# Optimization experiments

Hardware: AMD Instinct MI355X
Metric: run time of the kernel (lower is better)

Reference implementation:

```python
import jax, jax.numpy as jnp
import numpy as np
import math

B, T, S, D, H = 64, 128, 3, 1024, 8
DK = D // H  # 128


def setup_inputs() -> dict:
    key = jax.random.key(0)
    ks = jax.random.split(key, 12)
    sc = 0.02
    inputs = jax.random.normal(ks[0], (B, T, D), jnp.float32)
    # init_memory: identity over slots, zero-padded to d_model, flattened
    memory = jnp.broadcast_to(jnp.eye(S, D, dtype=jnp.float32), (B, S, D)).reshape(B, S * D)
    def lin(k, din, dout):
        return jax.random.normal(k, (din, dout), jnp.float32) * sc
    return {
        "inputs": inputs, "memory": memory,
        "Wq": lin(ks[1], D, D), "bq": jnp.zeros((D,), jnp.float32),
        "Wk": lin(ks[2], D, D), "bk": jnp.zeros((D,), jnp.float32),
        "Wv": lin(ks[3], D, D), "bv": jnp.zeros((D,), jnp.float32),
        "Wo": lin(ks[4], D, D), "bo": jnp.zeros((D,), jnp.float32),
        "W1": lin(ks[5], D, D), "b1": jnp.zeros((D,), jnp.float32),
        "W2": lin(ks[6], D, D), "b2": jnp.zeros((D,), jnp.float32),
        "Wg": lin(ks[7], D, 2 * D), "bg": jnp.zeros((2 * D,), jnp.float32),
        "Ug": lin(ks[8], D, 2 * D), "bu": jnp.zeros((2 * D,), jnp.float32),
    }


def reference(inputs, memory, Wq, bq, Wk, bk, Wv, bv, Wo, bo,
              W1, b1, W2, b2, Wg, bg, Ug, bu):
    scale = 1.0 / math.sqrt(DK)

    def step(mem_flat, x):  # mem_flat: [B, S*D], x: [B, D]
        mem = mem_flat.reshape(-1, S, D)
        kv = jnp.concatenate([mem, x[:, None, :]], axis=1)  # [B, S+1, D]
        q = (mem @ Wq + bq).reshape(-1, S, H, DK).transpose(0, 2, 1, 3)       # [B,H,S,DK]
        k = (kv @ Wk + bk).reshape(-1, S + 1, H, DK).transpose(0, 2, 1, 3)    # [B,H,S+1,DK]
        v = (kv @ Wv + bv).reshape(-1, S + 1, H, DK).transpose(0, 2, 1, 3)
        scores = jnp.einsum('bhqd,bhkd->bhqk', q, k) * scale
        p = jax.nn.softmax(scores, axis=-1)
        o = jnp.einsum('bhqk,bhkd->bhqd', p, v).transpose(0, 2, 1, 3).reshape(-1, S, D)
        attn = o @ Wo + bo
        nm = mem + attn
        ml = jax.nn.relu(jax.nn.relu(nm @ W1 + b1) @ W2 + b2)
        nm = nm + ml
        gates = x[:, None, :] @ Wg + bg + jnp.tanh(mem) @ Ug + bu  # [B,S,2D]
        ig, fg = jnp.split(gates, 2, axis=-1)
        nm = jax.nn.sigmoid(ig) * jnp.tanh(nm) + jax.nn.sigmoid(fg) * mem
        nm_flat = nm.reshape(-1, S * D)
        return nm_flat, nm_flat

    xs = jnp.swapaxes(inputs, 0, 1)  # [T, B, D]
    _, outs = jax.lax.scan(step, memory, xs)  # outs: [T, B, S*D]
    return jnp.swapaxes(outs, 0, 1)  # [B, T, S*D]
```

## Files before the change

kernel.cpp:

```cpp
#include <hip/hip_runtime.h>
#include <math.h>

#define T_ 128

__device__ __forceinline__ double sigm_d(double x) { return 1.0 / (1.0 + exp(-x)); }

template<int COLS, typename AT, class F>
__device__ __forceinline__ void tile_gemm_pf(double* __restrict__ As,
                                             float* __restrict__ Ws,
                                             const AT* __restrict__ A, long lda,
                                             const float* __restrict__ W, int ldw,
                                             int n_off, F f) {
  constexpr int CT = COLS / 16;
  constexpr int WP = COLS + 4;
  constexpr int RP = 256 / COLS;
  constexpr int WL = 64 / RP;
  const int tid = threadIdx.x;
  const int c0 = (tid & 15) * CT;
  const int r0 = (tid >> 4) * 2;
  const int ar = tid >> 3;
  const int ak = (tid & 7) * 8;
  const int wn = tid & (COLS - 1);
  const int wk = tid / COLS;

  double aReg[8];
  float  wReg[WL];
  {
    const AT* Ap = A + (size_t)ar * lda + ak;
#pragma unroll
    for (int i = 0; i < 8; ++i) aReg[i] = (double)Ap[i];
    const float* Wp = W + (size_t)wk * ldw + n_off + wn;
#pragma unroll
    for (int p = 0; p < WL; ++p) wReg[p] = Wp[(size_t)p * RP * ldw];
  }
  double acc[2][CT];
#pragma unroll
  for (int i = 0; i < 2; ++i)
#pragma unroll
    for (int j = 0; j < CT; ++j) acc[i][j] = 0.0;

  for (int k0 = 0; k0 < 1024; k0 += 64) {
#pragma unroll
    for (int i = 0; i < 8; ++i) As[ar * 65 + ak + i] = aReg[i];
#pragma unroll
    for (int p = 0; p < WL; ++p) Ws[(wk + p * RP) * WP + wn] = wReg[p];
    __syncthreads();
    if (k0 + 64 < 1024) {
      const AT* Ap = A + (size_t)ar * lda + (k0 + 64) + ak;
#pragma unroll
      for (int i = 0; i < 8; ++i) aReg[i] = (double)Ap[i];
      const float* Wp = W + (size_t)(k0 + 64 + wk) * ldw + n_off + wn;
#pragma unroll
      for (int p = 0; p < WL; ++p) wReg[p] = Wp[(size_t)p * RP * ldw];
    }
#pragma unroll
    for (int kk = 0; kk < 64; ++kk) {
      double a0 = As[r0 * 65 + kk], a1 = As[(r0 + 1) * 65 + kk];
      const float* wrow = Ws + kk * WP + c0;
#pragma unroll
      for (int j = 0; j < CT; ++j) {
        double w = (double)wrow[j];
        acc[0][j] = fma(a0, w, acc[0][j]);
        acc[1][j] = fma(a1, w, acc[1][j]);
      }
    }
    __syncthreads();
  }
#pragma unroll
  for (int i = 0; i < 2; ++i)
#pragma unroll
    for (int j = 0; j < CT; ++j) f(r0 + i, c0 + j, acc[i][j]);
}

__global__ __launch_bounds__(256) void k_init(const float* __restrict__ memory,
                                              double* __restrict__ mem,
                                              double* __restrict__ tmem, int n) {
  int i = blockIdx.x * 256 + threadIdx.x;
  if (i >= n) return;
  double v = (double)memory[i];
  mem[i] = v; tmem[i] = tanh(v);
}

__global__ __launch_bounds__(256, 4) void k_stepA(
    const double* __restrict__ mem, const double* __restrict__ tmem,
    const float* __restrict__ inputs,
    const float* __restrict__ Wq, const float* __restrict__ Wk,
    const float* __restrict__ Wv, const float* __restrict__ Ug,
    const float* __restrict__ Wg,
    const float* __restrict__ bq, const float* __restrict__ bk,
    const float* __restrict__ bv, const float* __restrict__ bg,
    const float* __restrict__ bu,
    float* __restrict__ q, float* __restrict__ km, float* __restrict__ vm,
    float* __restrict__ g, float* __restrict__ kx, float* __restrict__ vx,
    float* __restrict__ xg, int t) {
  __shared__ double As[32 * 65];
  __shared__ float  Ws[64 * 68];
  int bid = blockIdx.x;
  if (bid < 480) {
    int ct = bid / 6, rt = bid % 6;
    int cb = ct * 64, rb = rt * 32;
    const double* Asrc = ((cb < 3072) ? mem : tmem) + (size_t)rb * 1024;
    const float* W; int ldw, n_off;
    if      (cb < 1024) { W = Wq; ldw = 1024; n_off = cb; }
    else if (cb < 2048) { W = Wk; ldw = 1024; n_off = cb - 1024; }
    else if (cb < 3072) { W = Wv; ldw = 1024; n_off = cb - 2048; }
    else                { W = Ug; ldw = 2048; n_off = cb - 3072; }
    tile_gemm_pf<64>(As, Ws, Asrc, 1024L, W, ldw, n_off,
                     [&](int r, int c, double v) {
      int row = rb + r, col = cb + c;
      if (col < 1024)      q [(size_t)row * 1024 + col]        = (float)(v + (double)bq[col]);
      else if (col < 2048) km[(size_t)row * 1024 + col - 1024] = (float)(v + (double)bk[col - 1024]);
      else if (col < 3072) vm[(size_t)row * 1024 + col - 2048] = (float)(v + (double)bv[col - 2048]);
      else                 g [(size_t)row * 2048 + col - 3072] = (float)v;
    });
  } else {
    int pb = bid - 480;
    int ct = pb / 2, rt = pb % 2;
    int cb = ct * 64, rb = rt * 32;
    const float* Asrc = inputs + (size_t)rb * (T_ * 1024) + (size_t)t * 1024;
    const float* W; int ldw, n_off;
    if      (cb < 1024) { W = Wk; ldw = 1024; n_off = cb; }
    else if (cb < 2048) { W = Wv; ldw = 1024; n_off = cb - 1024; }
    else                { W = Wg; ldw = 2048; n_off = cb - 2048; }
    tile_gemm_pf<64>(As, Ws, Asrc, (long)T_ * 1024, W, ldw, n_off,
                     [&](int r, int c, double v) {
      int b = rb + r, col = cb + c;
      if (col < 1024)      kx[(size_t)b * 1024 + col]        = (float)(v + (double)bk[col]);
      else if (col < 2048) vx[(size_t)b * 1024 + col - 1024] = (float)(v + (double)bv[col - 1024]);
      else { int j = col - 2048; xg[(size_t)b * 2048 + j] = (float)(v + (double)bg[j] + (double)bu[j]); }
    });
  }
}

__global__ __launch_bounds__(64) void k_attn(const float* __restrict__ q,
                                             const float* __restrict__ km,
                                             const float* __restrict__ vm,
                                             const float* __restrict__ kx,
                                             const float* __restrict__ vx,
                                             double* __restrict__ o) {
  int bh = blockIdx.x; int b = bh >> 3, h = bh & 7;
  int lane = threadIdx.x;
  int col = h * 128 + lane;
  double q0[3], q1[3], kk0[4], kk1[4], vv0[4], vv1[4];
#pragma unroll
  for (int s = 0; s < 3; ++s) {
    size_t r = (size_t)(b * 3 + s) * 1024 + col;
    q0[s] = (double)q[r]; q1[s] = (double)q[r + 64];
  }
#pragma unroll
  for (int j = 0; j < 3; ++j) {
    size_t r = (size_t)(b * 3 + j) * 1024 + col;
    kk0[j] = (double)km[r]; kk1[j] = (double)km[r + 64];
    vv0[j] = (double)vm[r]; vv1[j] = (double)vm[r + 64];
  }
  {
    size_t r = (size_t)b * 1024 + col;
    kk0[3] = (double)kx[r]; kk1[3] = (double)kx[r + 64];
    vv0[3] = (double)vx[r]; vv1[3] = (double)vx[r + 64];
  }
  const double scale = 0.08838834764831845;
  double p[3][4];
#pragma unroll
  for (int s = 0; s < 3; ++s)
#pragma unroll
    for (int j = 0; j < 4; ++j) {
      double d = q0[s] * kk0[j] + q1[s] * kk1[j];
#pragma unroll
      for (int off = 32; off > 0; off >>= 1) d += __shfl_xor(d, off);
      p[s][j] = d * scale;
    }
#pragma unroll
  for (int s = 0; s < 3; ++s) {
    double m = fmax(fmax(p[s][0], p[s][1]), fmax(p[s][2], p[s][3]));
    double e0 = exp(p[s][0] - m), e1 = exp(p[s][1] - m);
    double e2 = exp(p[s][2] - m), e3 = exp(p[s][3] - m);
    double inv = 1.0 / (e0 + e1 + e2 + e3);
    double o0 = (e0 * vv0[0] + e1 * vv0[1] + e2 * vv0[2] + e3 * vv0[3]) * inv;
    double o1 = (e0 * vv1[0] + e1 * vv1[1] + e2 * vv1[2] + e3 * vv1[3]) * inv;
    size_t r = (size_t)(b * 3 + s) * 1024 + col;
    o[r] = o0; o[r + 64] = o1;
  }
}

__global__ __launch_bounds__(256) void k_attnout(const double* __restrict__ o,
                                                 const float* __restrict__ Wo,
                                                 const float* __restrict__ bo,
                                                 const double* __restrict__ mem,
                                                 double* __restrict__ nm) {
  __shared__ double As[32 * 65];
  __shared__ float  Ws[64 * 36];
  int ct = blockIdx.x / 6, rt = blockIdx.x % 6;
  int cb = ct * 32, rb = rt * 32;
  tile_gemm_pf<32>(As, Ws, o + (size_t)rb * 1024, 1024L, Wo, 1024, cb,
                   [&](int r, int c, double v) {
    size_t idx = (size_t)(rb + r) * 1024 + cb + c;
    nm[idx] = mem[idx] + v + (double)bo[cb + c];
  });
}

__global__ __launch_bounds__(256) void k_ff1(const double* __restrict__ nm,
                                             const float* __restrict__ W1,
                                             const float* __restrict__ b1,
                                             double* __restrict__ h1) {
  __shared__ double As[32 * 65];
  __shared__ float  Ws[64 * 36];
  int ct = blockIdx.x / 6, rt = blockIdx.x % 6;
  int cb = ct * 32, rb = rt * 32;
  tile_gemm_pf<32>(As, Ws, nm + (size_t)rb * 1024, 1024L, W1, 1024, cb,
                   [&](int r, int c, double v) {
    h1[(size_t)(rb + r) * 1024 + cb + c] = fmax(v + (double)b1[cb + c], 0.0);
  });
}

__global__ __launch_bounds__(256) void k_ff2gate(const double* __restrict__ h1,
                                                 const float* __restrict__ W2,
                                                 const float* __restrict__ b2,
                                                 const double* __restrict__ nm,
                                                 const float* __restrict__ xg,
                                                 const float* __restrict__ g,
                                                 double* __restrict__ mem,
                                                 double* __restrict__ tmem,
                                                 float* __restrict__ out, int t) {
  __shared__ double As[32 * 65];
  __shared__ float  Ws[64 * 36];
  int ct = blockIdx.x / 6, rt = blockIdx.x % 6;
  int cb = ct * 32, rb = rt * 32;
  tile_gemm_pf<32>(As, Ws, h1 + (size_t)rb * 1024, 1024L, W2, 1024, cb,
                   [&](int r, int c, double v) {
    int row = rb + r, col = cb + c;
    size_t idx = (size_t)row * 1024 + col;
    double ml = fmax(v + (double)b2[col], 0.0);
    double nm2 = nm[idx] + ml;
    int b = row / 3;
    int s = row - b * 3;
    double ig = (double)xg[(size_t)b * 2048 + col]        + (double)g[(size_t)row * 2048 + col];
    double fg = (double)xg[(size_t)b * 2048 + 1024 + col] + (double)g[(size_t)row * 2048 + 1024 + col];
    double old = mem[idx];
    double nv = sigm_d(ig) * tanh(nm2) + sigm_d(fg) * old;
    out[(size_t)(b * T_ + t) * 3072 + s * 1024 + col] = (float)nv;
    mem[idx]  = nv;
    tmem[idx] = tanh(nv);
  });
}

extern "C" void kernel_launch(void* const* d_in, const int* in_sizes, int n_in,
                              void* d_out, int out_size, void* d_ws, size_t ws_size,
                              hipStream_t stream) {
  (void)in_sizes; (void)n_in; (void)out_size;
  const float* inputs = (const float*)d_in[0];
  const float* memory = (const float*)d_in[1];
  const float* Wq = (const float*)d_in[2];  const float* bq = (const float*)d_in[3];
  const float* Wk = (const float*)d_in[4];  const float* bk = (const float*)d_in[5];
  const float* Wv = (const float*)d_in[6];  const float* bv = (const float*)d_in[7];
  const float* Wo = (const float*)d_in[8];  const float* bo = (const float*)d_in[9];
  const float* W1 = (const float*)d_in[10]; const float* b1 = (const float*)d_in[11];
  const float* W2 = (const float*)d_in[12]; const float* b2 = (const float*)d_in[13];
  const float* Wg = (const float*)d_in[14]; const float* bg = (const float*)d_in[15];
  const float* Ug = (const float*)d_in[16]; const float* bu = (const float*)d_in[17];
  float* out = (float*)d_out;

  if (ws_size < (size_t)16 * 1024 * 1024) return;

  char* ws = (char*)d_ws;
  size_t off = 0;
  auto alloc = [&](size_t bytes) -> void* {
    void* p = ws + off; off += (bytes + 255) & ~(size_t)255; return p;
  };
  double* mem  = (double*)alloc((size_t)196608 * 8);
  double* tmem = (double*)alloc((size_t)196608 * 8);
  double* nm   = (double*)alloc((size_t)196608 * 8);
  double* o    = (double*)alloc((size_t)196608 * 8);
  double* h1   = (double*)alloc((size_t)196608 * 8);
  float* q  = (float*)alloc((size_t)196608 * 4);
  float* km = (float*)alloc((size_t)196608 * 4);
  float* vm = (float*)alloc((size_t)196608 * 4);
  float* g  = (float*)alloc((size_t)192 * 2048 * 4);
  float* kx = (float*)alloc((size_t)64 * 1024 * 4);
  float* vx = (float*)alloc((size_t)64 * 1024 * 4);
  float* xg = (float*)alloc((size_t)64 * 2048 * 4);

  k_init<<<768, 256, 0, stream>>>(memory, mem, tmem, 196608);

  for (int t = 0; t < T_; ++t) {
    k_stepA<<<608, 256, 0, stream>>>(mem, tmem, inputs, Wq, Wk, Wv, Ug, Wg,
                                     bq, bk, bv, bg, bu,
                                     q, km, vm, g, kx, vx, xg, t);
    k_attn<<<512, 64, 0, stream>>>(q, km, vm, kx, vx, o);
    k_attnout<<<192, 256, 0, stream>>>(o, Wo, bo, mem, nm);
    k_ff1<<<192, 256, 0, stream>>>(nm, W1, b1, h1);
    k_ff2gate<<<192, 256, 0, stream>>>(h1, W2, b2, nm, xg, g, mem, tmem, out, t);
  }
}
```

Baseline: 28.50 ms.

## Fuse all per-timestep kernels into one persistent kernel with grid barriers

```diff
diff --git a/kernel.cpp b/kernel.cpp
--- a/kernel.cpp
+++ b/kernel.cpp
@@ -2,48 +2,59 @@
 #include <math.h>
 
 #define T_ 128
+#define NBLK 256
 
 __device__ __forceinline__ double sigm_d(double x) { return 1.0 / (1.0 + exp(-x)); }
 
-template<int COLS, typename AT, class F>
-__device__ __forceinline__ void tile_gemm_pf(double* __restrict__ As,
-                                             float* __restrict__ Ws,
-                                             const AT* __restrict__ A, long lda,
-                                             const float* __restrict__ W, int ldw,
-                                             int n_off, F f) {
-  constexpr int CT = COLS / 16;
-  constexpr int WP = COLS + 4;
-  constexpr int RP = 256 / COLS;
-  constexpr int WL = 64 / RP;
+__device__ __forceinline__ void gsync(unsigned* cnt, unsigned* gen) {
+  __threadfence();
+  __syncthreads();
+  if (threadIdx.x == 0) {
+    unsigned g = __hip_atomic_load(gen, __ATOMIC_RELAXED, __HIP_MEMORY_SCOPE_AGENT);
+    unsigned a = __hip_atomic_fetch_add(cnt, 1u, __ATOMIC_ACQ_REL, __HIP_MEMORY_SCOPE_AGENT);
+    if (a == NBLK - 1u) {
+      __hip_atomic_store(cnt, 0u, __ATOMIC_RELAXED, __HIP_MEMORY_SCOPE_AGENT);
+      __hip_atomic_store(gen, g + 1u, __ATOMIC_RELEASE, __HIP_MEMORY_SCOPE_AGENT);
+    } else {
+      while (__hip_atomic_load(gen, __ATOMIC_ACQUIRE, __HIP_MEMORY_SCOPE_AGENT) == g)
+        __builtin_amdgcn_s_sleep(1);
+    }
+  }
+  __syncthreads();
+}
+
+template<typename AT, class F>
+__device__ __forceinline__ void job_gemm(double* __restrict__ As,
+                                         float* __restrict__ Ws,
+                                         const AT* __restrict__ A, long lda,
+                                         const float* __restrict__ W, int ldw,
+                                         int n_off, F f) {
   const int tid = threadIdx.x;
-  const int c0 = (tid & 15) * CT;
+  const int c0 = (tid & 15) * 2;
   const int r0 = (tid >> 4) * 2;
   const int ar = tid >> 3;
   const int ak = (tid & 7) * 8;
-  const int wn = tid & (COLS - 1);
-  const int wk = tid / COLS;
+  const int wn = tid & 31;
+  const int wk = tid >> 5;
 
   double aReg[8];
-  float  wReg[WL];
+  float  wReg[8];
   {
     const AT* Ap = A + (size_t)ar * lda + ak;
 #pragma unroll
     for (int i = 0; i < 8; ++i) aReg[i] = (double)Ap[i];
     const float* Wp = W + (size_t)wk * ldw + n_off + wn;
 #pragma unroll
-    for (int p = 0; p < WL; ++p) wReg[p] = Wp[(size_t)p * RP * ldw];
-  }
-  double acc[2][CT];
-#pragma unroll
-  for (int i = 0; i < 2; ++i)
-#pragma unroll
-    for (int j = 0; j < CT; ++j) acc[i][j] = 0.0;
+    for (int p = 0; p < 8; ++p) wReg[p] = Wp[(size_t)p * 8 * ldw];
+  }
+  double acc[2][2];
+  acc[0][0] = acc[0][1] = acc[1][0] = acc[1][1] = 0.0;
 
   for (int k0 = 0; k0 < 1024; k0 += 64) {
 #pragma unroll
     for (int i = 0; i < 8; ++i) As[ar * 65 + ak + i] = aReg[i];
 #pragma unroll
-    for (int p = 0; p < WL; ++p) Ws[(wk + p * RP) * WP + wn] = wReg[p];
+    for (int p = 0; p < 8; ++p) Ws[(wk + p * 8) * 36 + wn] = wReg[p];
     __syncthreads();
     if (k0 + 64 < 1024) {
       const AT* Ap = A + (size_t)ar * lda + (k0 + 64) + ak;
@@ -51,196 +62,188 @@
       for (int i = 0; i < 8; ++i) aReg[i] = (double)Ap[i];
       const float* Wp = W + (size_t)(k0 + 64 + wk) * ldw + n_off + wn;
 #pragma unroll
-      for (int p = 0; p < WL; ++p) wReg[p] = Wp[(size_t)p * RP * ldw];
+      for (int p = 0; p < 8; ++p) wReg[p] = Wp[(size_t)p * 8 * ldw];
     }
 #pragma unroll
     for (int kk = 0; kk < 64; ++kk) {
       double a0 = As[r0 * 65 + kk], a1 = As[(r0 + 1) * 65 + kk];
-      const float* wrow = Ws + kk * WP + c0;
-#pragma unroll
-      for (int j = 0; j < CT; ++j) {
-        double w = (double)wrow[j];
-        acc[0][j] = fma(a0, w, acc[0][j]);
-        acc[1][j] = fma(a1, w, acc[1][j]);
-      }
+      double w0 = (double)Ws[kk * 36 + c0], w1 = (double)Ws[kk * 36 + c0 + 1];
+      acc[0][0] = fma(a0, w0, acc[0][0]);
+      acc[0][1] = fma(a0, w1, acc[0][1]);
+      acc[1][0] = fma(a1, w0, acc[1][0]);
+      acc[1][1] = fma(a1, w1, acc[1][1]);
     }
     __syncthreads();
   }
 #pragma unroll
   for (int i = 0; i < 2; ++i)
 #pragma unroll
-    for (int j = 0; j < CT; ++j) f(r0 + i, c0 + j, acc[i][j]);
+    for (int j = 0; j < 2; ++j) f(r0 + i, c0 + j, acc[i][j]);
 }
 
 __global__ __launch_bounds__(256) void k_init(const float* __restrict__ memory,
                                               double* __restrict__ mem,
-                                              double* __restrict__ tmem, int n) {
+                                              double* __restrict__ tmem,
+                                              unsigned* __restrict__ cnt,
+                                              unsigned* __restrict__ gen, int n) {
   int i = blockIdx.x * 256 + threadIdx.x;
+  if (i == 0) { *cnt = 0u; *gen = 0u; }
   if (i >= n) return;
   double v = (double)memory[i];
   mem[i] = v; tmem[i] = tanh(v);
 }
 
-__global__ __launch_bounds__(256, 4) void k_stepA(
-    const double* __restrict__ mem, const double* __restrict__ tmem,
+__global__ __launch_bounds__(256) void k_fused(
     const float* __restrict__ inputs,
     const float* __restrict__ Wq, const float* __restrict__ Wk,
-    const float* __restrict__ Wv, const float* __restrict__ Ug,
-    const float* __restrict__ Wg,
+    const float* __restrict__ Wv, const float* __restrict__ Wo,
+    const float* __restrict__ W1, const float* __restrict__ W2,
+    const float* __restrict__ Wg, const float* __restrict__ Ug,
     const float* __restrict__ bq, const float* __restrict__ bk,
-    const float* __restrict__ bv, const float* __restrict__ bg,
-    const float* __restrict__ bu,
+    const float* __restrict__ bv, const float* __restrict__ bo,
+    const float* __restrict__ b1, const float* __restrict__ b2,
+    const float* __restrict__ bg, const float* __restrict__ bu,
+    double* __restrict__ mem, double* __restrict__ tmem,
+    double* __restrict__ nm, double* __restrict__ o, double* __restrict__ h1,
     float* __restrict__ q, float* __restrict__ km, float* __restrict__ vm,
     float* __restrict__ g, float* __restrict__ kx, float* __restrict__ vx,
-    float* __restrict__ xg, int t) {
-  __shared__ double As[32 * 65];
-  __shared__ float  Ws[64 * 68];
-  int bid = blockIdx.x;
-  if (bid < 480) {
-    int ct = bid / 6, rt = bid % 6;
-    int cb = ct * 64, rb = rt * 32;
-    const double* Asrc = ((cb < 3072) ? mem : tmem) + (size_t)rb * 1024;
-    const float* W; int ldw, n_off;
-    if      (cb < 1024) { W = Wq; ldw = 1024; n_off = cb; }
-    else if (cb < 2048) { W = Wk; ldw = 1024; n_off = cb - 1024; }
-    else if (cb < 3072) { W = Wv; ldw = 1024; n_off = cb - 2048; }
-    else                { W = Ug; ldw = 2048; n_off = cb - 3072; }
-    tile_gemm_pf<64>(As, Ws, Asrc, 1024L, W, ldw, n_off,
-                     [&](int r, int c, double v) {
-      int row = rb + r, col = cb + c;
-      if (col < 1024)      q [(size_t)row * 1024 + col]        = (float)(v + (double)bq[col]);
-      else if (col < 2048) km[(size_t)row * 1024 + col - 1024] = (float)(v + (double)bk[col - 1024]);
-      else if (col < 3072) vm[(size_t)row * 1024 + col - 2048] = (float)(v + (double)bv[col - 2048]);
-      else                 g [(size_t)row * 2048 + col - 3072] = (float)v;
-    });
-  } else {
-    int pb = bid - 480;
-    int ct = pb / 2, rt = pb % 2;
-    int cb = ct * 64, rb = rt * 32;
-    const float* Asrc = inputs + (size_t)rb * (T_ * 1024) + (size_t)t * 1024;
-    const float* W; int ldw, n_off;
-    if      (cb < 1024) { W = Wk; ldw = 1024; n_off = cb; }
-    else if (cb < 2048) { W = Wv; ldw = 1024; n_off = cb - 1024; }
-    else                { W = Wg; ldw = 2048; n_off = cb - 2048; }
-    tile_gemm_pf<64>(As, Ws, Asrc, (long)T_ * 1024, W, ldw, n_off,
-                     [&](int r, int c, double v) {
-      int b = rb + r, col = cb + c;
-      if (col < 1024)      kx[(size_t)b * 1024 + col]        = (float)(v + (double)bk[col]);
-      else if (col < 2048) vx[(size_t)b * 1024 + col - 1024] = (float)(v + (double)bv[col - 1024]);
-      else { int j = col - 2048; xg[(size_t)b * 2048 + j] = (float)(v + (double)bg[j] + (double)bu[j]); }
-    });
-  }
-}
-
-__global__ __launch_bounds__(64) void k_attn(const float* __restrict__ q,
-                                             const float* __restrict__ km,
-                                             const float* __restrict__ vm,
-                                             const float* __restrict__ kx,
-                                             const float* __restrict__ vx,
-                                             double* __restrict__ o) {
-  int bh = blockIdx.x; int b = bh >> 3, h = bh & 7;
-  int lane = threadIdx.x;
-  int col = h * 128 + lane;
-  double q0[3], q1[3], kk0[4], kk1[4], vv0[4], vv1[4];
-#pragma unroll
-  for (int s = 0; s < 3; ++s) {
-    size_t r = (size_t)(b * 3 + s) * 1024 + col;
-    q0[s] = (double)q[r]; q1[s] = (double)q[r + 64];
-  }
-#pragma unroll
-  for (int j = 0; j < 3; ++j) {
-    size_t r = (size_t)(b * 3 + j) * 1024 + col;
-    kk0[j] = (double)km[r]; kk1[j] = (double)km[r + 64];
-    vv0[j] = (double)vm[r]; vv1[j] = (double)vm[r + 64];
-  }
-  {
-    size_t r = (size_t)b * 1024 + col;
-    kk0[3] = (double)kx[r]; kk1[3] = (double)kx[r + 64];
-    vv0[3] = (double)vx[r]; vv1[3] = (double)vx[r + 64];
-  }
-  const double scale = 0.08838834764831845;
-  double p[3][4];
-#pragma unroll
-  for (int s = 0; s < 3; ++s)
-#pragma unroll
-    for (int j = 0; j < 4; ++j) {
-      double d = q0[s] * kk0[j] + q1[s] * kk1[j];
-#pragma unroll
-      for (int off = 32; off > 0; off >>= 1) d += __shfl_xor(d, off);
-      p[s][j] = d * scale;
-    }
-#pragma unroll
-  for (int s = 0; s < 3; ++s) {
-    double m = fmax(fmax(p[s][0], p[s][1]), fmax(p[s][2], p[s][3]));
-    double e0 = exp(p[s][0] - m), e1 = exp(p[s][1] - m);
-    double e2 = exp(p[s][2] - m), e3 = exp(p[s][3] - m);
-    double inv = 1.0 / (e0 + e1 + e2 + e3);
-    double o0 = (e0 * vv0[0] + e1 * vv0[1] + e2 * vv0[2] + e3 * vv0[3]) * inv;
-    double o1 = (e0 * vv1[0] + e1 * vv1[1] + e2 * vv1[2] + e3 * vv1[3]) * inv;
-    size_t r = (size_t)(b * 3 + s) * 1024 + col;
-    o[r] = o0; o[r + 64] = o1;
-  }
-}
-
-__global__ __launch_bounds__(256) void k_attnout(const double* __restrict__ o,
-                                                 const float* __restrict__ Wo,
-                                                 const float* __restrict__ bo,
-                                                 const double* __restrict__ mem,
-                                                 double* __restrict__ nm) {
+    float* __restrict__ xg,
+    unsigned* __restrict__ cnt, unsigned* __restrict__ gen,
+    float* __restrict__ out) {
   __shared__ double As[32 * 65];
   __shared__ float  Ws[64 * 36];
-  int ct = blockIdx.x / 6, rt = blockIdx.x % 6;
-  int cb = ct * 32, rb = rt * 32;
-  tile_gemm_pf<32>(As, Ws, o + (size_t)rb * 1024, 1024L, Wo, 1024, cb,
-                   [&](int r, int c, double v) {
-    size_t idx = (size_t)(rb + r) * 1024 + cb + c;
-    nm[idx] = mem[idx] + v + (double)bo[cb + c];
-  });
-}
-
-__global__ __launch_bounds__(256) void k_ff1(const double* __restrict__ nm,
-                                             const float* __restrict__ W1,
-                                             const float* __restrict__ b1,
-                                             double* __restrict__ h1) {
-  __shared__ double As[32 * 65];
-  __shared__ float  Ws[64 * 36];
-  int ct = blockIdx.x / 6, rt = blockIdx.x % 6;
-  int cb = ct * 32, rb = rt * 32;
-  tile_gemm_pf<32>(As, Ws, nm + (size_t)rb * 1024, 1024L, W1, 1024, cb,
-                   [&](int r, int c, double v) {
-    h1[(size_t)(rb + r) * 1024 + cb + c] = fmax(v + (double)b1[cb + c], 0.0);
-  });
-}
-
-__global__ __launch_bounds__(256) void k_ff2gate(const double* __restrict__ h1,
-                                                 const float* __restrict__ W2,
-                                                 const float* __restrict__ b2,
-                                                 const double* __restrict__ nm,
-                                                 const float* __restrict__ xg,
-                                                 const float* __restrict__ g,
-                                                 double* __restrict__ mem,
-                                                 double* __restrict__ tmem,
-                                                 float* __restrict__ out, int t) {
-  __shared__ double As[32 * 65];
-  __shared__ float  Ws[64 * 36];
-  int ct = blockIdx.x / 6, rt = blockIdx.x % 6;
-  int cb = ct * 32, rb = rt * 32;
-  tile_gemm_pf<32>(As, Ws, h1 + (size_t)rb * 1024, 1024L, W2, 1024, cb,
-                   [&](int r, int c, double v) {
-    int row = rb + r, col = cb + c;
-    size_t idx = (size_t)row * 1024 + col;
-    double ml = fmax(v + (double)b2[col], 0.0);
-    double nm2 = nm[idx] + ml;
-    int b = row / 3;
-    int s = row - b * 3;
-    double ig = (double)xg[(size_t)b * 2048 + col]        + (double)g[(size_t)row * 2048 + col];
-    double fg = (double)xg[(size_t)b * 2048 + 1024 + col] + (double)g[(size_t)row * 2048 + 1024 + col];
-    double old = mem[idx];
-    double nv = sigm_d(ig) * tanh(nm2) + sigm_d(fg) * old;
-    out[(size_t)(b * T_ + t) * 3072 + s * 1024 + col] = (float)nv;
-    mem[idx]  = nv;
-    tmem[idx] = tanh(nv);
-  });
+  const int blk = blockIdx.x;
+  const int tid = threadIdx.x;
+
+  for (int t = 0; t < T_; ++t) {
+    for (int j = blk; j < 1216; j += NBLK) {
+      if (j < 960) {
+        int ct = j / 6, rt = j % 6;
+        int cb = ct * 32, rb = rt * 32;
+        const double* Asrc = ((cb < 3072) ? mem : tmem) + (size_t)rb * 1024;
+        const float* W; int ldw, n_off;
+        if      (cb < 1024) { W = Wq; ldw = 1024; n_off = cb; }
+        else if (cb < 2048) { W = Wk; ldw = 1024; n_off = cb - 1024; }
+        else if (cb < 3072) { W = Wv; ldw = 1024; n_off = cb - 2048; }
+        else                { W = Ug; ldw = 2048; n_off = cb - 3072; }
+        job_gemm(As, Ws, Asrc, 1024L, W, ldw, n_off,
+                 [&](int r, int c, double v) {
+          int row = rb + r, col = cb + c;
+          if (col < 1024)      q [(size_t)row * 1024 + col]        = (float)(v + (double)bq[col]);
+          else if (col < 2048) km[(size_t)row * 1024 + col - 1024] = (float)(v + (double)bk[col - 1024]);
+          else if (col < 3072) vm[(size_t)row * 1024 + col - 2048] = (float)(v + (double)bv[col - 2048]);
+          else                 g [(size_t)row * 2048 + col - 3072] = (float)v;
+        });
+      } else {
+        int pb = j - 960;
+        int ct = pb / 2, rt = pb % 2;
+        int cb = ct * 32, rb = rt * 32;
+        const float* Asrc = inputs + (size_t)rb * (T_ * 1024) + (size_t)t * 1024;
+        const float* W; int ldw, n_off;
+        if      (cb < 1024) { W = Wk; ldw = 1024; n_off = cb; }
+        else if (cb < 2048) { W = Wv; ldw = 1024; n_off = cb - 1024; }
+        else                { W = Wg; ldw = 2048; n_off = cb - 2048; }
+        job_gemm(As, Ws, Asrc, (long)T_ * 1024, W, ldw, n_off,
+                 [&](int r, int c, double v) {
+          int b = rb + r, col = cb + c;
+          if (col < 1024)      kx[(size_t)b * 1024 + col]        = (float)(v + (double)bk[col]);
+          else if (col < 2048) vx[(size_t)b * 1024 + col - 1024] = (float)(v + (double)bv[col - 1024]);
+          else { int jj = col - 2048; xg[(size_t)b * 2048 + jj] = (float)(v + (double)bg[jj] + (double)bu[jj]); }
+        });
+      }
+    }
+    gsync(cnt, gen);
+
+    if (blk < 128) {
+      int bh = blk * 4 + (tid >> 6);
+      int b = bh >> 3, h = bh & 7;
+      int lane = tid & 63;
+      int col = h * 128 + lane;
+      double q0[3], q1[3], kk0[4], kk1[4], vv0[4], vv1[4];
+#pragma unroll
+      for (int s = 0; s < 3; ++s) {
+        size_t r = (size_t)(b * 3 + s) * 1024 + col;
+        q0[s] = (double)q[r]; q1[s] = (double)q[r + 64];
+      }
+#pragma unroll
+      for (int j = 0; j < 3; ++j) {
+        size_t r = (size_t)(b * 3 + j) * 1024 + col;
+        kk0[j] = (double)km[r]; kk1[j] = (double)km[r + 64];
+        vv0[j] = (double)vm[r]; vv1[j] = (double)vm[r + 64];
+      }
+      {
+        size_t r = (size_t)b * 1024 + col;
+        kk0[3] = (double)kx[r]; kk1[3] = (double)kx[r + 64];
+        vv0[3] = (double)vx[r]; vv1[3] = (double)vx[r + 64];
+      }
+      const double scale = 0.08838834764831845;
+      double p[3][4];
+#pragma unroll
+      for (int s = 0; s < 3; ++s)
+#pragma unroll
+        for (int j = 0; j < 4; ++j) {
+          double d = q0[s] * kk0[j] + q1[s] * kk1[j];
+#pragma unroll
+          for (int off = 32; off > 0; off >>= 1) d += __shfl_xor(d, off);
+          p[s][j] = d * scale;
+        }
+#pragma unroll
+      for (int s = 0; s < 3; ++s) {
+        double m = fmax(fmax(p[s][0], p[s][1]), fmax(p[s][2], p[s][3]));
+        double e0 = exp(p[s][0] - m), e1 = exp(p[s][1] - m);
+        double e2 = exp(p[s][2] - m), e3 = exp(p[s][3] - m);
+        double inv = 1.0 / (e0 + e1 + e2 + e3);
+        double o0 = (e0 * vv0[0] + e1 * vv0[1] + e2 * vv0[2] + e3 * vv0[3]) * inv;
+        double o1 = (e0 * vv1[0] + e1 * vv1[1] + e2 * vv1[2] + e3 * vv1[3]) * inv;
+        size_t r = (size_t)(b * 3 + s) * 1024 + col;
+        o[r] = o0; o[r + 64] = o1;
+      }
+    }
+    gsync(cnt, gen);
+
+    if (blk < 192) {
+      int ct = blk / 6, rt = blk % 6;
+      int cb = ct * 32, rb = rt * 32;
+      job_gemm(As, Ws, o + (size_t)rb * 1024, 1024L, Wo, 1024, cb,
+               [&](int r, int c, double v) {
+        size_t idx = (size_t)(rb + r) * 1024 + cb + c;
+        nm[idx] = mem[idx] + v + (double)bo[cb + c];
+      });
+    }
+    gsync(cnt, gen);
+
+    if (blk < 192) {
+      int ct = blk / 6, rt = blk % 6;
+      int cb = ct * 32, rb = rt * 32;
+      job_gemm(As, Ws, nm + (size_t)rb * 1024, 1024L, W1, 1024, cb,
+               [&](int r, int c, double v) {
+        h1[(size_t)(rb + r) * 1024 + cb + c] = fmax(v + (double)b1[cb + c], 0.0);
+      });
+    }
+    gsync(cnt, gen);
+
+    if (blk < 192) {
+      int ct = blk / 6, rt = blk % 6;
+      int cb = ct * 32, rb = rt * 32;
+      job_gemm(As, Ws, h1 + (size_t)rb * 1024, 1024L, W2, 1024, cb,
+               [&](int r, int c, double v) {
+        int row = rb + r, col = cb + c;
+        size_t idx = (size_t)row * 1024 + col;
+        double ml = fmax(v + (double)b2[col], 0.0);
+        double nm2 = nm[idx] + ml;
+        int b = row / 3;
+        int s = row - b * 3;
+        double ig = (double)xg[(size_t)b * 2048 + col]        + (double)g[(size_t)row * 2048 + col];
+        double fg = (double)xg[(size_t)b * 2048 + 1024 + col] + (double)g[(size_t)row * 2048 + 1024 + col];
+        double old = mem[idx];
+        double nv = sigm_d(ig) * tanh(nm2) + sigm_d(fg) * old;
+        out[(size_t)(b * T_ + t) * 3072 + s * 1024 + col] = (float)nv;
+        mem[idx]  = nv;
+        tmem[idx] = tanh(nv);
+      });
+    }
+    gsync(cnt, gen);
+  }
 }
 
 extern "C" void kernel_launch(void* const* d_in, const int* in_sizes, int n_in,
@@ -266,6 +269,8 @@
   auto alloc = [&](size_t bytes) -> void* {
     void* p = ws + off; off += (bytes + 255) & ~(size_t)255; return p;
   };
+  unsigned* cnt = (unsigned*)alloc(256);
+  unsigned* gen = (unsigned*)alloc(256);
   double* mem  = (double*)alloc((size_t)196608 * 8);
   double* tmem = (double*)alloc((size_t)196608 * 8);
   double* nm   = (double*)alloc((size_t)196608 * 8);
@@ -279,15 +284,9 @@
   float* vx = (float*)alloc((size_t)64 * 1024 * 4);
   float* xg = (float*)alloc((size_t)64 * 2048 * 4);
 
-  k_init<<<768, 256, 0, stream>>>(memory, mem, tmem, 196608);
-
-  for (int t = 0; t < T_; ++t) {
-    k_stepA<<<608, 256, 0, stream>>>(mem, tmem, inputs, Wq, Wk, Wv, Ug, Wg,
-                                     bq, bk, bv, bg, bu,
-                                     q, km, vm, g, kx, vx, xg, t);
-    k_attn<<<512, 64, 0, stream>>>(q, km, vm, kx, vx, o);
-    k_attnout<<<192, 256, 0, stream>>>(o, Wo, bo, mem, nm);
-    k_ff1<<<192, 256, 0, stream>>>(nm, W1, b1, h1);
-    k_ff2gate<<<192, 256, 0, stream>>>(h1, W2, b2, nm, xg, g, mem, tmem, out, t);
-  }
-}
+  k_init<<<768, 256, 0, stream>>>(memory, mem, tmem, cnt, gen, 196608);
+  k_fused<<<NBLK, 256, 0, stream>>>(inputs, Wq, Wk, Wv, Wo, W1, W2, Wg, Ug,
+                                    bq, bk, bv, bo, b1, b2, bg, bu,
+                                    mem, tmem, nm, o, h1,
+                                    q, km, vm, g, kx, vx, xg, cnt, gen, out);
+}
```

New measurement: 72.81 ms. +155.5%, slower.
